# Kernel optimization log

Measured on AMD Instinct MI355X. Metric: run time of the kernel, lower is better.

The kernel has to match this reference:

```python
import jax, jax.numpy as jnp
import numpy as np

T, IN, H, OUT, L = 2048, 128, 128, 128, 2


def setup_inputs() -> dict:
    key = jax.random.key(0)
    ks = jax.random.split(key, 12)
    s_in = 1.0 / np.sqrt(IN)
    s_h = 1.0 / np.sqrt(H)
    s_ff = 1.0 / np.sqrt(2 * H)
    return {
        "emb": jax.random.normal(ks[0], (T, IN), jnp.float32),
        "start": jax.random.randint(ks[1], (T,), 0, 2).astype(jnp.int32),
        "w_in": jax.random.normal(ks[2], (H, IN), jnp.float32) * s_in,
        "b_in": jnp.zeros((H,), jnp.float32),
        "w_out": jax.random.normal(ks[3], (OUT, H), jnp.float32) * s_h,
        "b_out": jnp.zeros((OUT,), jnp.float32),
        "w_f": jax.random.normal(ks[4], (L, 1, H), jnp.float32) * s_h,
        "b_f": jnp.zeros((L, 1), jnp.float32),
        "w_i": jax.random.normal(ks[5], (L, 1, H), jnp.float32) * s_h,
        "b_i": jnp.zeros((L, 1), jnp.float32),
        "w_v": jax.random.normal(ks[6], (L, H, H), jnp.float32) * s_h,
        "b_v": jnp.zeros((L, H), jnp.float32),
        "w_q": jax.random.normal(ks[7], (L, H, H), jnp.float32) * s_h,
        "b_q": jnp.zeros((L, H), jnp.float32),
        "w_k": jax.random.normal(ks[8], (L, H, H), jnp.float32) * s_h,
        "b_k": jnp.zeros((L, H), jnp.float32),
        "w_o": jax.random.normal(ks[9], (L, H, H), jnp.float32) * s_h,
        "b_o": jnp.zeros((L, H), jnp.float32),
        "w_ff": jax.random.normal(ks[10], (L, H, 2 * H), jnp.float32) * s_ff,
        "b_ff": jnp.zeros((L, H), jnp.float32),
    }


def _mlstm_layer(x, gate_mask, w_f, b_f, w_i, b_i, w_v, b_v, w_q, b_q, w_k, b_k, w_o, b_o):
    # x: [T, H] layer input; gate_mask: [T] (0.0 at episode starts -> reset)
    Hdim = x.shape[-1]
    i = jnp.exp(x @ w_i.T + b_i)                           # [T, 1] exp input gate
    v = x @ w_v.T + b_v                                    # [T, H]
    k = (x * (1.0 / np.sqrt(Hdim))) @ w_k.T + b_k          # [T, H] (1/sqrt(H) applied before Linear)
    C = i[:, :, None] * (v[:, :, None] * k[:, None, :])    # [T, H, H] gated outer products
    n = i * k                                              # [T, H]
    g = jax.nn.sigmoid(x @ w_f.T + b_f)[:, 0] * gate_mask  # [T] forget gate, zeroed at resets

    def step(carry, inp):
        S, m = carry
        Ct, nt, gt = inp
        S = gt * S + Ct
        m = gt * m + nt
        return (S, m), (S, m)

    init = (jnp.zeros((Hdim, Hdim), x.dtype), jnp.zeros((Hdim,), x.dtype))
    _, (S_all, m_all) = jax.lax.scan(step, init, (C, n, g))  # [T,H,H], [T,H]

    q = x @ w_q.T + b_q                                    # [T, H]
    o = jax.nn.sigmoid(x @ w_o.T + b_o)                    # [T, H]
    num = jnp.einsum('thk,tk->th', S_all, q)               # C @ q per step
    den = jnp.maximum(jnp.abs(jnp.einsum('th,th->t', m_all, q))[:, None], 1.0)
    return o * (num / den)


def reference(emb, start, w_in, b_in, w_out, b_out, w_f, b_f, w_i, b_i,
              w_v, b_v, w_q, b_q, w_k, b_k, w_o, b_o, w_ff, b_ff):
    gate_mask = 1.0 - start.astype(emb.dtype)              # reset => discard previous state
    e = emb @ w_in.T + b_in                                # [T, H]
    z = e
    for l in range(w_f.shape[0]):
        h = _mlstm_layer(z, gate_mask, w_f[l], b_f[l], w_i[l], b_i[l],
                         w_v[l], b_v[l], w_q[l], b_q[l], w_k[l], b_k[l], w_o[l], b_o[l])
        z = jax.nn.leaky_relu(jnp.concatenate([h, e], axis=-1) @ w_ff[l].T + b_ff[l])
    return z @ w_out.T + b_out
```

## Files before the change

kernel.cpp:

```cpp
#include <hip/hip_runtime.h>
#include <math.h>

#define TT 2048
#define HH 128
#define ROWS 8
#define SP 132

__device__ __forceinline__ float dot4(float4 a, float4 b) {
    return a.x * b.x + a.y * b.y + a.z * b.z + a.w * b.w;
}

__global__ __launch_bounds__(256) void prep_kernel(
        const float* __restrict__ w_in, const float* __restrict__ w_out,
        const float* __restrict__ w_v, const float* __restrict__ w_q,
        const float* __restrict__ w_k, const float* __restrict__ w_o,
        const float* __restrict__ w_ff,
        float4* __restrict__ win_p, float4* __restrict__ wout_p,
        float4* __restrict__ wcat, float4* __restrict__ wff_p) {
    int i = blockIdx.x * 256 + threadIdx.x;
    if (i < 4096) {
        int cg = i >> 7, col = i & 127;
        win_p[i] = ((const float4*)w_in)[col * 32 + cg];
    } else if (i < 8192) {
        int j = i - 4096, cg = j >> 7, col = j & 127;
        wout_p[j] = ((const float4*)w_out)[col * 32 + cg];
    } else if (i < 40960) {
        int j = i - 8192;
        int l = j >> 14, r = j & 16383, cg = r >> 9, col = r & 511;
        int sel = col >> 7, cm = col & 127;
        const float* s = (sel == 0 ? w_v : sel == 1 ? w_q : sel == 2 ? w_k : w_o) + l * HH * HH;
        wcat[j] = ((const float4*)s)[cm * 32 + cg];
    } else {
        int j = i - 40960;
        int l = j >> 13, r = j & 8191, cg = r >> 7, col = r & 127;
        const float* s = w_ff + l * HH * 256;
        wff_p[j] = ((const float4*)s)[col * 64 + cg];
    }
}

__device__ __forceinline__ void attn_row(int t0,
        const float* __restrict__ kb, const float* __restrict__ vb,
        const float* __restrict__ qb, const float* __restrict__ ob,
        const float* __restrict__ g, const float* __restrict__ iexp,
        float* __restrict__ hs) {
    int tid = threadIdx.x;
    int wv = tid >> 6, lane = tid & 63;
    int t = t0 + wv;
    float2 q2 = *(const float2*)(qb + t * HH + 2 * lane);
    float2 o2 = *(const float2*)(ob + t * HH + 2 * lane);
    int tp = t;
    float2 k2 = *(const float2*)(kb + tp * HH + 2 * lane);
    float2 v2 = *(const float2*)(vb + tp * HH + 2 * lane);
    float ie = iexp[tp], gv = g[tp];
    float nx = 0.f, ny = 0.f, dsum = 0.f, decay = 1.f;
    while (true) {
        bool cont = (tp > 0) && (gv != 0.f);
        float2 k2n = {0.f, 0.f}, v2n = {0.f, 0.f};
        float ien = 0.f, gvn = 0.f;
        if (cont) {
            k2n = *(const float2*)(kb + (tp - 1) * HH + 2 * lane);
            v2n = *(const float2*)(vb + (tp - 1) * HH + 2 * lane);
            ien = iexp[tp - 1]; gvn = g[tp - 1];
        }
        float p = k2.x * q2.x + k2.y * q2.y;
#pragma unroll
        for (int off = 1; off <= 32; off <<= 1) p += __shfl_xor(p, off, 64);
        float coeff = decay * ie * p;
        nx += coeff * v2.x; ny += coeff * v2.y; dsum += coeff;
        if (!cont) break;
        decay *= gv;
        tp--; k2 = k2n; v2 = v2n; ie = ien; gv = gvn;
    }
    float inv = 1.f / fmaxf(fabsf(dsum), 1.f);
    *(float2*)(hs + wv * SP + 2 * lane) = make_float2(o2.x * nx * inv, o2.y * ny * inv);
}

__device__ __forceinline__ void proj_fi(int t0, const float* __restrict__ xls,
        const float* __restrict__ w_f, const float* __restrict__ b_f,
        const float* __restrict__ w_i, const float* __restrict__ b_i,
        const int* __restrict__ start, float* __restrict__ g, float* __restrict__ iexp) {
    int tid = threadIdx.x;
    int wv = tid >> 6, lane = tid & 63;
    const float* x = xls + wv * SP + 2 * lane;
    float pf = x[0] * w_f[2 * lane] + x[1] * w_f[2 * lane + 1];
    float pi = x[0] * w_i[2 * lane] + x[1] * w_i[2 * lane + 1];
#pragma unroll
    for (int off = 1; off <= 32; off <<= 1) {
        pf += __shfl_xor(pf, off, 64);
        pi += __shfl_xor(pi, off, 64);
    }
    if (lane == 0) {
        int t = t0 + wv;
        g[t] = start[t] ? 0.f : 1.f / (1.f + expf(-(pf + b_f[0])));
        iexp[t] = expf(pi + b_i[0]);
    }
}

__device__ __forceinline__ void proj_block(int t0, const float* __restrict__ xls,
        const float4* __restrict__ wcat,
        const float* __restrict__ b_v, const float* __restrict__ b_q,
        const float* __restrict__ b_k, const float* __restrict__ b_o,
        float* __restrict__ vb, float* __restrict__ qb,
        float* __restrict__ kb, float* __restrict__ ob) {
    int tid = threadIdx.x;
    int col = tid, mat = tid >> 7, cm = tid & 127;
    float acc[8] = {0.f, 0.f, 0.f, 0.f, 0.f, 0.f, 0.f, 0.f};
#pragma unroll 8
    for (int cg = 0; cg < 32; ++cg) {
        float4 w4 = wcat[cg * 512 + col];
#pragma unroll
        for (int r = 0; r < 8; ++r) {
            float4 x4 = *(const float4*)(xls + r * SP + 4 * cg);
            acc[r] += dot4(x4, w4);
        }
    }
    const float ks = 0.088388347648318447f;
    const float* bsel = mat == 0 ? b_v : mat == 1 ? b_q : mat == 2 ? b_k : b_o;
    float* dst = mat == 0 ? vb : mat == 1 ? qb : mat == 2 ? kb : ob;
    float bb = bsel[cm];
#pragma unroll
    for (int r = 0; r < 8; ++r) {
        float a = acc[r];
        if (mat == 2) a *= ks;
        a += bb;
        if (mat == 3) a = 1.f / (1.f + expf(-a));
        dst[(t0 + r) * HH + cm] = a;
    }
}

__device__ __forceinline__ void ff_block(const float* __restrict__ hsb,
        const float* __restrict__ esb, const float4* __restrict__ wff,
        const float* __restrict__ b_ff, float* __restrict__ zs) {
    int tid = threadIdx.x;
    int col = tid & 127, rg = tid >> 7;
    int r0 = 2 * rg, r1 = r0 + 1;
    float a0 = 0.f, a1 = 0.f;
#pragma unroll 8
    for (int cg = 0; cg < 32; ++cg) {
        float4 w4 = wff[cg * 128 + col];
        a0 += dot4(*(const float4*)(hsb + r0 * SP + 4 * cg), w4);
        a1 += dot4(*(const float4*)(hsb + r1 * SP + 4 * cg), w4);
    }
#pragma unroll 8
    for (int cg = 32; cg < 64; ++cg) {
        float4 w4 = wff[cg * 128 + col];
        int c = 4 * (cg - 32);
        a0 += dot4(*(const float4*)(esb + r0 * SP + c), w4);
        a1 += dot4(*(const float4*)(esb + r1 * SP + c), w4);
    }
    float bb = b_ff[col];
    a0 += bb; a1 += bb;
    a0 = a0 > 0.f ? a0 : 0.01f * a0;
    a1 = a1 > 0.f ? a1 : 0.01f * a1;
    zs[r0 * SP + col] = a0;
    zs[r1 * SP + col] = a1;
}

__device__ __forceinline__ void dense128(int t0, const float* __restrict__ xls,
        const float4* __restrict__ Wp, const float* __restrict__ b,
        float* __restrict__ yg, float* __restrict__ ys) {
    int tid = threadIdx.x;
    int col = tid & 127, rg = tid >> 7;
    int r0 = 2 * rg, r1 = r0 + 1;
    float a0 = 0.f, a1 = 0.f;
#pragma unroll 8
    for (int cg = 0; cg < 32; ++cg) {
        float4 w4 = Wp[cg * 128 + col];
        a0 += dot4(*(const float4*)(xls + r0 * SP + 4 * cg), w4);
        a1 += dot4(*(const float4*)(xls + r1 * SP + 4 * cg), w4);
    }
    float bb = b[col];
    a0 += bb; a1 += bb;
    yg[(t0 + r0) * HH + col] = a0;
    yg[(t0 + r1) * HH + col] = a1;
    if (ys) {
        ys[r0 * SP + col] = a0;
        ys[r1 * SP + col] = a1;
    }
}

__global__ __launch_bounds__(512, 2) void k1_kernel(
        const float* __restrict__ emb, const int* __restrict__ start,
        const float4* __restrict__ win_p, const float* __restrict__ b_in,
        const float4* __restrict__ wcat0,
        const float* __restrict__ b_v, const float* __restrict__ b_q,
        const float* __restrict__ b_k, const float* __restrict__ b_o,
        const float* __restrict__ w_f, const float* __restrict__ b_f,
        const float* __restrict__ w_i, const float* __restrict__ b_i,
        float* __restrict__ e, float* __restrict__ kb, float* __restrict__ vb,
        float* __restrict__ qb, float* __restrict__ ob,
        float* __restrict__ g, float* __restrict__ iexp) {
    __shared__ float xs[ROWS * SP];
    __shared__ float es[ROWS * SP];
    int tid = threadIdx.x;
    int t0 = blockIdx.x * ROWS;
    int wv = tid >> 6, lane = tid & 63;
    *(float2*)(xs + wv * SP + 2 * lane) = *(const float2*)(emb + (t0 + wv) * HH + 2 * lane);
    __syncthreads();
    dense128(t0, xs, win_p, b_in, e, es);
    __syncthreads();
    proj_block(t0, es, wcat0, b_v, b_q, b_k, b_o, vb, qb, kb, ob);
    proj_fi(t0, es, w_f, b_f, w_i, b_i, start, g, iexp);
}

__global__ __launch_bounds__(512, 2) void k2_kernel(
        const int* __restrict__ start, const float* __restrict__ e,
        const float* __restrict__ k0, const float* __restrict__ v0,
        const float* __restrict__ q0, const float* __restrict__ o0,
        const float* __restrict__ g0, const float* __restrict__ i0,
        const float4* __restrict__ wff0, const float* __restrict__ b_ff,
        const float4* __restrict__ wcat1,
        const float* __restrict__ b_v, const float* __restrict__ b_q,
        const float* __restrict__ b_k, const float* __restrict__ b_o,
        const float* __restrict__ w_f, const float* __restrict__ b_f,
        const float* __restrict__ w_i, const float* __restrict__ b_i,
        float* __restrict__ kb, float* __restrict__ vb,
        float* __restrict__ qb, float* __restrict__ ob,
        float* __restrict__ g, float* __restrict__ iexp) {
    __shared__ float es[ROWS * SP];
    __shared__ float hs[ROWS * SP];
    __shared__ float zs[ROWS * SP];
    int tid = threadIdx.x;
    int t0 = blockIdx.x * ROWS;
    int wv = tid >> 6, lane = tid & 63;
    float2 ev = *(const float2*)(e + (t0 + wv) * HH + 2 * lane);
    attn_row(t0, k0, v0, q0, o0, g0, i0, hs);
    *(float2*)(es + wv * SP + 2 * lane) = ev;
    __syncthreads();
    ff_block(hs, es, wff0, b_ff, zs);
    __syncthreads();
    proj_block(t0, zs, wcat1, b_v, b_q, b_k, b_o, vb, qb, kb, ob);
    proj_fi(t0, zs, w_f, b_f, w_i, b_i, start, g, iexp);
}

__global__ __launch_bounds__(512, 2) void k3_kernel(
        const float* __restrict__ e,
        const float* __restrict__ k1, const float* __restrict__ v1,
        const float* __restrict__ q1, const float* __restrict__ o1,
        const float* __restrict__ g1, const float* __restrict__ i1,
        const float4* __restrict__ wff1, const float* __restrict__ b_ff,
        const float4* __restrict__ wout_p, const float* __restrict__ b_out,
        float* __restrict__ out) {
    __shared__ float es[ROWS * SP];
    __shared__ float hs[ROWS * SP];
    __shared__ float zs[ROWS * SP];
    int tid = threadIdx.x;
    int t0 = blockIdx.x * ROWS;
    int wv = tid >> 6, lane = tid & 63;
    float2 ev = *(const float2*)(e + (t0 + wv) * HH + 2 * lane);
    attn_row(t0, k1, v1, q1, o1, g1, i1, hs);
    *(float2*)(es + wv * SP + 2 * lane) = ev;
    __syncthreads();
    ff_block(hs, es, wff1, b_ff, zs);
    __syncthreads();
    dense128(t0, zs, wout_p, b_out, out, (float*)0);
}

extern "C" void kernel_launch(void* const* d_in, const int* in_sizes, int n_in,
                              void* d_out, int out_size, void* d_ws, size_t ws_size,
                              hipStream_t stream) {
    const float* emb   = (const float*)d_in[0];
    const int*   start = (const int*)  d_in[1];
    const float* w_in  = (const float*)d_in[2];
    const float* b_in  = (const float*)d_in[3];
    const float* w_out = (const float*)d_in[4];
    const float* b_out = (const float*)d_in[5];
    const float* w_f   = (const float*)d_in[6];
    const float* b_f   = (const float*)d_in[7];
    const float* w_i   = (const float*)d_in[8];
    const float* b_i   = (const float*)d_in[9];
    const float* w_v   = (const float*)d_in[10];
    const float* b_v   = (const float*)d_in[11];
    const float* w_q   = (const float*)d_in[12];
    const float* b_q   = (const float*)d_in[13];
    const float* w_k   = (const float*)d_in[14];
    const float* b_k   = (const float*)d_in[15];
    const float* w_o   = (const float*)d_in[16];
    const float* b_o   = (const float*)d_in[17];
    const float* w_ff  = (const float*)d_in[18];
    const float* b_ff  = (const float*)d_in[19];
    float* out = (float*)d_out;

    float* ws = (float*)d_ws;
    float* e   = ws; ws += TT * HH;
    float* k0b = ws; ws += TT * HH;
    float* v0b = ws; ws += TT * HH;
    float* q0b = ws; ws += TT * HH;
    float* o0b = ws; ws += TT * HH;
    float* k1b = ws; ws += TT * HH;
    float* v1b = ws; ws += TT * HH;
    float* q1b = ws; ws += TT * HH;
    float* o1b = ws; ws += TT * HH;
    float* g0  = ws; ws += TT;
    float* i0  = ws; ws += TT;
    float* g1  = ws; ws += TT;
    float* i1  = ws; ws += TT;
    float4* win_p  = (float4*)ws; ws += 16384;
    float4* wout_p = (float4*)ws; ws += 16384;
    float4* wcat   = (float4*)ws; ws += 131072;
    float4* wff_p  = (float4*)ws; ws += 65536;

    dim3 grid(TT / ROWS), block(512);
    prep_kernel<<<dim3(224), dim3(256), 0, stream>>>(
        w_in, w_out, w_v, w_q, w_k, w_o, w_ff, win_p, wout_p, wcat, wff_p);
    k1_kernel<<<grid, block, 0, stream>>>(
        emb, start, win_p, b_in, wcat,
        b_v, b_q, b_k, b_o, w_f, b_f, w_i, b_i,
        e, k0b, v0b, q0b, o0b, g0, i0);
    k2_kernel<<<grid, block, 0, stream>>>(
        start, e, k0b, v0b, q0b, o0b, g0, i0,
        wff_p, b_ff,
        wcat + 16384,
        b_v + HH, b_q + HH, b_k + HH, b_o + HH,
        w_f + HH, b_f + 1, w_i + HH, b_i + 1,
        k1b, v1b, q1b, o1b, g1, i1);
    k3_kernel<<<grid, block, 0, stream>>>(
        e, k1b, v1b, q1b, o1b, g1, i1,
        wff_p + 8192, b_ff + HH, wout_p, b_out, out);
}
```

Baseline: 152.2 us.

## Fuse three layer kernels into one persistent kernel with grid barriers

Merges k1/k2/k3 into one mega kernel of 256 blocks that synchronise through atomic-counter grid barriers. q, o and e stay in shared memory instead of round-tripping through global buffers, which removes two kernel launches and several global writes and reads. The barrier assumes every block is co-resident (256 blocks of 512 threads at two per CU), and a memset is added to clear the counters.

Result: slower. 176.1 us (+15.7%).

```diff
diff --git a/kernel.cpp b/kernel.cpp
--- a/kernel.cpp
+++ b/kernel.cpp
@@ -5,6 +5,7 @@
 #define HH 128
 #define ROWS 8
 #define SP 132
+#define NBLK (TT / ROWS)
 
 __device__ __forceinline__ float dot4(float4 a, float4 b) {
     return a.x * b.x + a.y * b.y + a.z * b.z + a.w * b.w;
@@ -38,16 +39,30 @@
     }
 }
 
+__device__ __forceinline__ void grid_barrier(unsigned* __restrict__ ctr) {
+    __syncthreads();
+    if (threadIdx.x == 0) {
+        __threadfence();
+        atomicAdd(ctr, 1u);
+        while (__hip_atomic_load(ctr, __ATOMIC_RELAXED, __HIP_MEMORY_SCOPE_AGENT)
+               < (unsigned)NBLK) {
+            __builtin_amdgcn_s_sleep(8);
+        }
+        __threadfence();
+    }
+    __syncthreads();
+}
+
 __device__ __forceinline__ void attn_row(int t0,
         const float* __restrict__ kb, const float* __restrict__ vb,
-        const float* __restrict__ qb, const float* __restrict__ ob,
+        const float* __restrict__ qs, const float* __restrict__ os,
         const float* __restrict__ g, const float* __restrict__ iexp,
         float* __restrict__ hs) {
     int tid = threadIdx.x;
     int wv = tid >> 6, lane = tid & 63;
     int t = t0 + wv;
-    float2 q2 = *(const float2*)(qb + t * HH + 2 * lane);
-    float2 o2 = *(const float2*)(ob + t * HH + 2 * lane);
+    float2 q2 = *(const float2*)(qs + wv * SP + 2 * lane);
+    float2 o2 = *(const float2*)(os + wv * SP + 2 * lane);
     int tp = t;
     float2 k2 = *(const float2*)(kb + tp * HH + 2 * lane);
     float2 v2 = *(const float2*)(vb + tp * HH + 2 * lane);
@@ -100,8 +115,8 @@
         const float4* __restrict__ wcat,
         const float* __restrict__ b_v, const float* __restrict__ b_q,
         const float* __restrict__ b_k, const float* __restrict__ b_o,
-        float* __restrict__ vb, float* __restrict__ qb,
-        float* __restrict__ kb, float* __restrict__ ob) {
+        float* __restrict__ kb, float* __restrict__ vb,
+        float* __restrict__ qs, float* __restrict__ os) {
     int tid = threadIdx.x;
     int col = tid, mat = tid >> 7, cm = tid & 127;
     float acc[8] = {0.f, 0.f, 0.f, 0.f, 0.f, 0.f, 0.f, 0.f};
@@ -115,16 +130,22 @@
         }
     }
     const float ks = 0.088388347648318447f;
-    const float* bsel = mat == 0 ? b_v : mat == 1 ? b_q : mat == 2 ? b_k : b_o;
-    float* dst = mat == 0 ? vb : mat == 1 ? qb : mat == 2 ? kb : ob;
-    float bb = bsel[cm];
-#pragma unroll
-    for (int r = 0; r < 8; ++r) {
-        float a = acc[r];
-        if (mat == 2) a *= ks;
-        a += bb;
-        if (mat == 3) a = 1.f / (1.f + expf(-a));
-        dst[(t0 + r) * HH + cm] = a;
+    if (mat == 0) {
+        float bb = b_v[cm];
+#pragma unroll
+        for (int r = 0; r < 8; ++r) vb[(t0 + r) * HH + cm] = acc[r] + bb;
+    } else if (mat == 1) {
+        float bb = b_q[cm];
+#pragma unroll
+        for (int r = 0; r < 8; ++r) qs[r * SP + cm] = acc[r] + bb;
+    } else if (mat == 2) {
+        float bb = b_k[cm];
+#pragma unroll
+        for (int r = 0; r < 8; ++r) kb[(t0 + r) * HH + cm] = acc[r] * ks + bb;
+    } else {
+        float bb = b_o[cm];
+#pragma unroll
+        for (int r = 0; r < 8; ++r) os[r * SP + cm] = 1.f / (1.f + expf(-(acc[r] + bb)));
     }
 }
 
@@ -171,87 +192,62 @@
     }
     float bb = b[col];
     a0 += bb; a1 += bb;
-    yg[(t0 + r0) * HH + col] = a0;
-    yg[(t0 + r1) * HH + col] = a1;
+    if (yg) {
+        yg[(t0 + r0) * HH + col] = a0;
+        yg[(t0 + r1) * HH + col] = a1;
+    }
     if (ys) {
         ys[r0 * SP + col] = a0;
         ys[r1 * SP + col] = a1;
     }
 }
 
-__global__ __launch_bounds__(512, 2) void k1_kernel(
+__global__ __launch_bounds__(512, 2) void mega_kernel(
         const float* __restrict__ emb, const int* __restrict__ start,
         const float4* __restrict__ win_p, const float* __restrict__ b_in,
-        const float4* __restrict__ wcat0,
+        const float4* __restrict__ wcat,
         const float* __restrict__ b_v, const float* __restrict__ b_q,
         const float* __restrict__ b_k, const float* __restrict__ b_o,
         const float* __restrict__ w_f, const float* __restrict__ b_f,
         const float* __restrict__ w_i, const float* __restrict__ b_i,
-        float* __restrict__ e, float* __restrict__ kb, float* __restrict__ vb,
-        float* __restrict__ qb, float* __restrict__ ob,
-        float* __restrict__ g, float* __restrict__ iexp) {
+        const float4* __restrict__ wff_p, const float* __restrict__ b_ff,
+        const float4* __restrict__ wout_p, const float* __restrict__ b_out,
+        float* __restrict__ k0b, float* __restrict__ v0b,
+        float* __restrict__ k1b, float* __restrict__ v1b,
+        float* __restrict__ g0, float* __restrict__ i0,
+        float* __restrict__ g1, float* __restrict__ i1,
+        unsigned* __restrict__ bar,
+        float* __restrict__ out) {
     __shared__ float xs[ROWS * SP];
-    __shared__ float es[ROWS * SP];
-    int tid = threadIdx.x;
-    int t0 = blockIdx.x * ROWS;
-    int wv = tid >> 6, lane = tid & 63;
-    *(float2*)(xs + wv * SP + 2 * lane) = *(const float2*)(emb + (t0 + wv) * HH + 2 * lane);
-    __syncthreads();
-    dense128(t0, xs, win_p, b_in, e, es);
-    __syncthreads();
-    proj_block(t0, es, wcat0, b_v, b_q, b_k, b_o, vb, qb, kb, ob);
-    proj_fi(t0, es, w_f, b_f, w_i, b_i, start, g, iexp);
-}
-
-__global__ __launch_bounds__(512, 2) void k2_kernel(
-        const int* __restrict__ start, const float* __restrict__ e,
-        const float* __restrict__ k0, const float* __restrict__ v0,
-        const float* __restrict__ q0, const float* __restrict__ o0,
-        const float* __restrict__ g0, const float* __restrict__ i0,
-        const float4* __restrict__ wff0, const float* __restrict__ b_ff,
-        const float4* __restrict__ wcat1,
-        const float* __restrict__ b_v, const float* __restrict__ b_q,
-        const float* __restrict__ b_k, const float* __restrict__ b_o,
-        const float* __restrict__ w_f, const float* __restrict__ b_f,
-        const float* __restrict__ w_i, const float* __restrict__ b_i,
-        float* __restrict__ kb, float* __restrict__ vb,
-        float* __restrict__ qb, float* __restrict__ ob,
-        float* __restrict__ g, float* __restrict__ iexp) {
     __shared__ float es[ROWS * SP];
     __shared__ float hs[ROWS * SP];
     __shared__ float zs[ROWS * SP];
+    __shared__ float qs[ROWS * SP];
+    __shared__ float os[ROWS * SP];
     int tid = threadIdx.x;
     int t0 = blockIdx.x * ROWS;
     int wv = tid >> 6, lane = tid & 63;
-    float2 ev = *(const float2*)(e + (t0 + wv) * HH + 2 * lane);
-    attn_row(t0, k0, v0, q0, o0, g0, i0, hs);
-    *(float2*)(es + wv * SP + 2 * lane) = ev;
-    __syncthreads();
-    ff_block(hs, es, wff0, b_ff, zs);
-    __syncthreads();
-    proj_block(t0, zs, wcat1, b_v, b_q, b_k, b_o, vb, qb, kb, ob);
-    proj_fi(t0, zs, w_f, b_f, w_i, b_i, start, g, iexp);
-}
-
-__global__ __launch_bounds__(512, 2) void k3_kernel(
-        const float* __restrict__ e,
-        const float* __restrict__ k1, const float* __restrict__ v1,
-        const float* __restrict__ q1, const float* __restrict__ o1,
-        const float* __restrict__ g1, const float* __restrict__ i1,
-        const float4* __restrict__ wff1, const float* __restrict__ b_ff,
-        const float4* __restrict__ wout_p, const float* __restrict__ b_out,
-        float* __restrict__ out) {
-    __shared__ float es[ROWS * SP];
-    __shared__ float hs[ROWS * SP];
-    __shared__ float zs[ROWS * SP];
-    int tid = threadIdx.x;
-    int t0 = blockIdx.x * ROWS;
-    int wv = tid >> 6, lane = tid & 63;
-    float2 ev = *(const float2*)(e + (t0 + wv) * HH + 2 * lane);
-    attn_row(t0, k1, v1, q1, o1, g1, i1, hs);
-    *(float2*)(es + wv * SP + 2 * lane) = ev;
-    __syncthreads();
-    ff_block(hs, es, wff1, b_ff, zs);
+
+    *(float2*)(xs + wv * SP + 2 * lane) = *(const float2*)(emb + (t0 + wv) * HH + 2 * lane);
+    __syncthreads();
+    dense128(t0, xs, win_p, b_in, (float*)0, es);
+    __syncthreads();
+    proj_block(t0, es, wcat, b_v, b_q, b_k, b_o, k0b, v0b, qs, os);
+    proj_fi(t0, es, w_f, b_f, w_i, b_i, start, g0, i0);
+    grid_barrier(bar + 0);
+
+    attn_row(t0, k0b, v0b, qs, os, g0, i0, hs);
+    __syncthreads();
+    ff_block(hs, es, wff_p, b_ff, zs);
+    __syncthreads();
+    proj_block(t0, zs, wcat + 16384, b_v + HH, b_q + HH, b_k + HH, b_o + HH,
+               k1b, v1b, qs, os);
+    proj_fi(t0, zs, w_f + HH, b_f + 1, w_i + HH, b_i + 1, start, g1, i1);
+    grid_barrier(bar + 1);
+
+    attn_row(t0, k1b, v1b, qs, os, g1, i1, hs);
+    __syncthreads();
+    ff_block(hs, es, wff_p + 8192, b_ff + HH, zs);
     __syncthreads();
     dense128(t0, zs, wout_p, b_out, out, (float*)0);
 }
@@ -281,16 +277,12 @@
     const float* b_ff  = (const float*)d_in[19];
     float* out = (float*)d_out;
 
-    float* ws = (float*)d_ws;
-    float* e   = ws; ws += TT * HH;
+    unsigned* bar = (unsigned*)d_ws;
+    float* ws = (float*)d_ws + 64;
     float* k0b = ws; ws += TT * HH;
     float* v0b = ws; ws += TT * HH;
-    float* q0b = ws; ws += TT * HH;
-    float* o0b = ws; ws += TT * HH;
     float* k1b = ws; ws += TT * HH;
     float* v1b = ws; ws += TT * HH;
-    float* q1b = ws; ws += TT * HH;
-    float* o1b = ws; ws += TT * HH;
     float* g0  = ws; ws += TT;
     float* i0  = ws; ws += TT;
     float* g1  = ws; ws += TT;
@@ -300,21 +292,13 @@
     float4* wcat   = (float4*)ws; ws += 131072;
     float4* wff_p  = (float4*)ws; ws += 65536;
 
-    dim3 grid(TT / ROWS), block(512);
+    hipMemsetAsync(bar, 0, 64, stream);
     prep_kernel<<<dim3(224), dim3(256), 0, stream>>>(
         w_in, w_out, w_v, w_q, w_k, w_o, w_ff, win_p, wout_p, wcat, wff_p);
-    k1_kernel<<<grid, block, 0, stream>>>(
+    mega_kernel<<<dim3(NBLK), dim3(512), 0, stream>>>(
         emb, start, win_p, b_in, wcat,
         b_v, b_q, b_k, b_o, w_f, b_f, w_i, b_i,
-        e, k0b, v0b, q0b, o0b, g0, i0);
-    k2_kernel<<<grid, block, 0, stream>>>(
-        start, e, k0b, v0b, q0b, o0b, g0, i0,
-        wff_p, b_ff,
-        wcat + 16384,
-        b_v + HH, b_q + HH, b_k + HH, b_o + HH,
-        w_f + HH, b_f + 1, w_i + HH, b_i + 1,
-        k1b, v1b, q1b, o1b, g1, i1);
-    k3_kernel<<<grid, block, 0, stream>>>(
-        e, k1b, v1b, q1b, o1b, g1, i1,
-        wff_p + 8192, b_ff + HH, wout_p, b_out, out);
-}
+        wff_p, b_ff, wout_p, b_out,
+        k0b, v0b, k1b, v1b, g0, i0, g1, i1,
+        bar, out);
+}
```
